# Kernel optimization log

Measured on AMD Instinct MI355X. Metric: run time of the kernel, lower is better.

The kernel has to match this reference:

```python
import jax, jax.numpy as jnp
import numpy as np

B, S, D = 2, 2048, 1024
H = 16
DH = D // H  # 64


def setup_inputs() -> dict:
    key = jax.random.key(0)
    ks = jax.random.split(key, 5)
    scale = 0.02
    x = jax.random.normal(ks[0], (B, S, D), dtype=jnp.float32)
    W_qkv = jax.random.normal(ks[1], (D, 3 * D), dtype=jnp.float32) * scale
    b_qkv = jnp.zeros((3 * D,), dtype=jnp.float32)
    W_out = jax.random.normal(ks[2], (D, D), dtype=jnp.float32) * scale
    b_out = jnp.zeros((D,), dtype=jnp.float32)
    return {"x": x, "W_qkv": W_qkv, "b_qkv": b_qkv, "W_out": W_out, "b_out": b_out}


def reference(x, W_qkv, b_qkv, W_out, b_out):
    # Fused QKV projection: [B,S,D] @ [D,3D] -> [B,S,3D]
    qkv = jnp.einsum('bsd,df->bsf', x, W_qkv) + b_qkv
    q, k, v = qkv[:, :, :D], qkv[:, :, D:2 * D], qkv[:, :, 2 * D:]
    # Split heads: [B,S,D] -> [B,H,S,DH]
    def split(t):
        return t.reshape(B, S, H, DH).transpose(0, 2, 1, 3)
    q, k, v = split(q), split(k), split(v)
    # Scaled dot-product attention (naive, full score matrix as in source)
    scores = jnp.einsum('bhqd,bhkd->bhqk', q, k) / jnp.sqrt(jnp.float32(DH))
    probs = jax.nn.softmax(scores, axis=-1)  # mask=None, dropout eval-mode identity
    attn = jnp.einsum('bhqk,bhkd->bhqd', probs, v)
    # Merge heads: [B,H,S,DH] -> [B,S,D]
    attn = attn.transpose(0, 2, 1, 3).reshape(B, S, D)
    out = jnp.einsum('bsd,de->bse', attn, W_out) + b_out
    return out
```

## Files before the change

### kernel.cpp

```cpp
#include <hip/hip_runtime.h>

typedef _Float16 half8  __attribute__((ext_vector_type(8)));
typedef _Float16 half4  __attribute__((ext_vector_type(4)));
typedef float    floatx4  __attribute__((ext_vector_type(4)));
typedef float    floatx16 __attribute__((ext_vector_type(16)));
typedef unsigned int uint4v __attribute__((ext_vector_type(4)));

constexpr int B_ = 2, S_ = 2048, D_ = 1024, H_ = 16, M_ = 4096;
constexpr int NR_ = B_ * H_ * S_;
constexpr float QSCALE = 0.18033688011112042f;
constexpr int KVB = 64;
constexpr int HT = 16;

__device__ __forceinline__ void gload16(const void* g, void* l) {
  __builtin_amdgcn_global_load_lds((const __attribute__((address_space(1))) void*)g,
                                   (__attribute__((address_space(3))) void*)l, 16, 0, 0);
}

__global__ __launch_bounds__(256) void cast_f32_f16(const float* __restrict__ in,
                                                    _Float16* __restrict__ out, int n8) {
  int i = blockIdx.x * 256 + threadIdx.x;
  if (i >= n8) return;
  float4 a = reinterpret_cast<const float4*>(in)[2 * i];
  float4 b = reinterpret_cast<const float4*>(in)[2 * i + 1];
  half8 h;
  h[0] = (_Float16)a.x; h[1] = (_Float16)a.y; h[2] = (_Float16)a.z; h[3] = (_Float16)a.w;
  h[4] = (_Float16)b.x; h[5] = (_Float16)b.y; h[6] = (_Float16)b.z; h[7] = (_Float16)b.w;
  reinterpret_cast<half8*>(out)[i] = h;
}

__global__ __launch_bounds__(256) void transpose_cast2(const float* __restrict__ W0,
                                                       _Float16* __restrict__ WT0,
                                                       const float* __restrict__ W1,
                                                       _Float16* __restrict__ WT1) {
  __shared__ float Ws[64][65];
  const int z = blockIdx.z;
  const int NW = z ? D_ : 3 * D_;
  if (blockIdx.x * 64 >= NW) return;
  const float* W = z ? W1 : W0;
  _Float16* WT = z ? WT1 : WT0;
  const int K = D_, N = NW;
  const int n0 = blockIdx.x * 64, k0 = blockIdx.y * 64;
  const int t = threadIdx.x;
#pragma unroll
  for (int i = 0; i < 4; i++) {
    int idx = t + 256 * i;
    int r = idx >> 4, c4 = idx & 15;
    float4 v = *reinterpret_cast<const float4*>(W + (size_t)(k0 + r) * N + n0 + c4 * 4);
    Ws[r][c4 * 4 + 0] = v.x; Ws[r][c4 * 4 + 1] = v.y;
    Ws[r][c4 * 4 + 2] = v.z; Ws[r][c4 * 4 + 3] = v.w;
  }
  __syncthreads();
#pragma unroll
  for (int i = 0; i < 2; i++) {
    int idx = t + 256 * i;
    int r = idx >> 3, ck = idx & 7;
    half8 h;
#pragma unroll
    for (int j = 0; j < 8; j++) h[j] = (_Float16)Ws[ck * 8 + j][r];
    *reinterpret_cast<half8*>(WT + (size_t)(n0 + r) * K + k0 + ck * 8) = h;
  }
}

__global__ __launch_bounds__(512, 2) void gemm256_mfma(
    const _Float16* __restrict__ A, const _Float16* __restrict__ BT,
    const float* __restrict__ bias, _Float16* __restrict__ Cout,
    _Float16* __restrict__ Vt,
    int M, int N, int K, float scale_lo, int ncut) {
  extern __shared__ char smem[];
  const int tid = threadIdx.x, w = tid >> 6, lane = tid & 63;
  const int wm = w >> 1, wn = w & 1;

  const int nwg = gridDim.x, cpx = nwg >> 3;
  const int wg = (blockIdx.x & 7) * cpx + (blockIdx.x >> 3);
  const int nbx = N / 192;
  const int bx = wg % nbx, by = wg / nbx;
  const int m0 = by * 256, n0 = bx * 192;

  const int NT = K >> 6;

  const int rS = tid >> 3, cS = (tid & 7) ^ (rS & 7);
  const char* Apn = (const char*)(A + (size_t)(m0 + rS) * K + cS * 8);
  const char* Bpn = (const char*)(BT + (size_t)(n0 + rS) * K + cS * 8);
  const size_t strideI = (size_t)64 * K * 2;

  auto stageA1 = [&](int buf, int i) {
    gload16(Apn + i * strideI, smem + buf * 32768 + tid * 16 + i * 8192);
  };
  auto stageB1 = [&](int buf, int i) {
    gload16(Bpn + i * strideI, smem + 65536 + buf * 24576 + tid * 16 + i * 8192);
  };

  floatx4 acc[4][6] = {};

#pragma unroll
  for (int i = 0; i < 4; i++) stageA1(0, i);
#pragma unroll
  for (int i = 0; i < 3; i++) stageB1(0, i);
  Apn += 128; Bpn += 128;

  for (int kt = 0; kt < NT; ++kt) {
    const int p = kt & 1;
    asm volatile("s_waitcnt vmcnt(0)" ::: "memory");
    __builtin_amdgcn_s_barrier();
    __builtin_amdgcn_sched_barrier(0);

    const char* Ab = smem + p * 32768;
    const char* Bb = smem + 65536 + p * 24576;
    const bool more = (kt + 1 < NT);

    half8 bf[6][2];
#pragma unroll
    for (int n = 0; n < 6; n++)
#pragma unroll
      for (int ks = 0; ks < 2; ks++) {
        int row = wn * 96 + n * 16 + (lane & 15);
        int ch = (ks * 4 + (lane >> 4)) ^ (row & 7);
        bf[n][ks] = *reinterpret_cast<const half8*>(Bb + row * 128 + ch * 16);
      }

#pragma unroll
    for (int q = 0; q < 4; q++) {
      half8 af[2];
#pragma unroll
      for (int ks = 0; ks < 2; ks++) {
        int row = wm * 64 + q * 16 + (lane & 15);
        int ch = (ks * 4 + (lane >> 4)) ^ (row & 7);
        af[ks] = *reinterpret_cast<const half8*>(Ab + row * 128 + ch * 16);
      }
      if (more) {
        if (q == 0)      { stageA1(p ^ 1, 0); stageA1(p ^ 1, 1); }
        else if (q == 1) { stageA1(p ^ 1, 2); stageA1(p ^ 1, 3); }
        else if (q == 2) { stageB1(p ^ 1, 0); stageB1(p ^ 1, 1); }
        else             { stageB1(p ^ 1, 2); }
      }
      __builtin_amdgcn_s_setprio(1);
#pragma unroll
      for (int ks = 0; ks < 2; ks++)
#pragma unroll
        for (int n = 0; n < 6; n++)
          acc[q][n] = __builtin_amdgcn_mfma_f32_16x16x32_f16(
              af[ks], bf[n][ks], acc[q][n], 0, 0, 0);
      __builtin_amdgcn_s_setprio(0);
    }
    Apn += 128; Bpn += 128;
    __builtin_amdgcn_sched_barrier(0);
    __builtin_amdgcn_s_barrier();
  }

#pragma unroll
  for (int mf = 0; mf < 4; mf++)
#pragma unroll
    for (int n = 0; n < 6; n++) {
      int col = n0 + wn * 96 + n * 16 + (lane & 15);
      float bv = bias[col];
      float sc = (col < ncut) ? scale_lo : 1.0f;
      int row0 = m0 + wm * 64 + mf * 16 + (lane >> 4) * 4;
      half4 hv;
#pragma unroll
      for (int reg = 0; reg < 4; reg++) {
        float v = (acc[mf][n][reg] + bv) * sc;
        _Float16 hvv = (_Float16)v;
        Cout[(size_t)(row0 + reg) * N + col] = hvv;
        hv[reg] = hvv;
      }
      if (col >= 2 * D_) {
        int d = col - 2 * D_;
        int bb = row0 >> 11, s0 = row0 & 2047;
        _Float16* vt = Vt + ((size_t)(bb * H_ + (d >> 6)) * 64 + (d & 63)) * S_ + s0;
        *reinterpret_cast<half4*>(vt) = hv;
      }
    }
}

__global__ __launch_bounds__(256, 2) void gemm128_mfma(
    const _Float16* __restrict__ A, const _Float16* __restrict__ BT,
    const float* __restrict__ bias, float* __restrict__ Cout,
    int M, int N, int K) {
  extern __shared__ char smem[];
  const int tid = threadIdx.x, w = tid >> 6, lane = tid & 63;
  const int wm = w >> 1, wn = w & 1;

  const int nwg = gridDim.x, cpx = nwg >> 3;
  const int wg = (blockIdx.x & 7) * cpx + (blockIdx.x >> 3);
  const int nbx = N >> 7;
  const int bx = wg % nbx, by = wg / nbx;
  const int m0 = by * 128, n0 = bx * 128;

  const int NT = K >> 6;

  const int rS = tid >> 3, cS = (tid & 7) ^ (rS & 7);
  const char* Apn = (const char*)(A + (size_t)(m0 + rS) * K + cS * 8);
  const char* Bpn = (const char*)(BT + (size_t)(n0 + rS) * K + cS * 8);
  const size_t strideI = (size_t)32 * K * 2;

  auto stageA1 = [&](int buf, int i) {
    gload16(Apn + i * strideI, smem + buf * 16384 + tid * 16 + i * 4096);
  };
  auto stageB1 = [&](int buf, int i) {
    gload16(Bpn + i * strideI, smem + 32768 + buf * 16384 + tid * 16 + i * 4096);
  };

  floatx4 acc[4][4] = {};

#pragma unroll
  for (int i = 0; i < 4; i++) stageA1(0, i);
#pragma unroll
  for (int i = 0; i < 4; i++) stageB1(0, i);
  Apn += 128; Bpn += 128;

  for (int kt = 0; kt < NT; ++kt) {
    const int p = kt & 1;
    asm volatile("s_waitcnt vmcnt(0)" ::: "memory");
    __builtin_amdgcn_s_barrier();
    __builtin_amdgcn_sched_barrier(0);

    const char* Ab = smem + p * 16384;
    const char* Bb = smem + 32768 + p * 16384;
    const bool more = (kt + 1 < NT);

    half8 bf[4][2];
#pragma unroll
    for (int n = 0; n < 4; n++)
#pragma unroll
      for (int ks = 0; ks < 2; ks++) {
        int row = wn * 64 + n * 16 + (lane & 15);
        int ch = (ks * 4 + (lane >> 4)) ^ (row & 7);
        bf[n][ks] = *reinterpret_cast<const half8*>(Bb + row * 128 + ch * 16);
      }

#pragma unroll
    for (int q = 0; q < 4; q++) {
      half8 af[2];
#pragma unroll
      for (int ks = 0; ks < 2; ks++) {
        int row = wm * 64 + q * 16 + (lane & 15);
        int ch = (ks * 4 + (lane >> 4)) ^ (row & 7);
        af[ks] = *reinterpret_cast<const half8*>(Ab + row * 128 + ch * 16);
      }
      if (more) {
        if (q == 0)      { stageA1(p ^ 1, 0); stageA1(p ^ 1, 1); }
        else if (q == 1) { stageA1(p ^ 1, 2); stageA1(p ^ 1, 3); }
        else if (q == 2) { stageB1(p ^ 1, 0); stageB1(p ^ 1, 1); }
        else             { stageB1(p ^ 1, 2); stageB1(p ^ 1, 3); }
      }
      __builtin_amdgcn_s_setprio(1);
#pragma unroll
      for (int ks = 0; ks < 2; ks++)
#pragma unroll
        for (int n = 0; n < 4; n++)
          acc[q][n] = __builtin_amdgcn_mfma_f32_16x16x32_f16(
              af[ks], bf[n][ks], acc[q][n], 0, 0, 0);
      __builtin_amdgcn_s_setprio(0);
    }
    Apn += 128; Bpn += 128;
    __builtin_amdgcn_sched_barrier(0);
    __builtin_amdgcn_s_barrier();
  }

#pragma unroll
  for (int q = 0; q < 4; q++)
#pragma unroll
    for (int n = 0; n < 4; n++) {
      int col = n0 + wn * 64 + n * 16 + (lane & 15);
      float bv = bias[col];
#pragma unroll
      for (int reg = 0; reg < 4; reg++) {
        int row = m0 + wm * 64 + q * 16 + (lane >> 4) * 4 + reg;
        Cout[(size_t)row * N + col] = acc[q][n][reg] + bv;
      }
    }
}

__global__ __launch_bounds__(256, 4) void flash_mfma(const _Float16* __restrict__ qkv,
                                                     const _Float16* __restrict__ Vt,
                                                     _Float16* __restrict__ Opart,
                                                     float* __restrict__ keys) {
  const int qt = blockIdx.x, h = blockIdx.y;
  const int b = blockIdx.z >> 1, sp = blockIdx.z & 1;
  const int t = threadIdx.x, w = t >> 6, lane = t & 63;
  const int lo = lane & 31, hi = lane >> 5;

  __shared__ _Float16 Ks[2][KVB * 64];
  __shared__ _Float16 Vts[2][64 * KVB];

  const int qrow = qt * 128 + w * 32 + lo;
  const _Float16* qbase = qkv + (size_t)(b * S_ + qrow) * (3 * D_) + h * 64;
  half8 qf[4];
#pragma unroll
  for (int kd = 0; kd < 4; kd++)
    qf[kd] = *reinterpret_cast<const half8*>(qbase + kd * 16 + hi * 8);
  asm volatile("" : "+v"(qf[0]), "+v"(qf[1]), "+v"(qf[2]), "+v"(qf[3]));

  const size_t kbase = (size_t)(b * S_) * (3 * D_) + D_ + h * 64;
  const size_t vbase = (size_t)(b * H_ + h) * 64 * S_;
  const int kvbase = sp * (S_ / 2);

  const int rs = t >> 3, cs = (t & 7) ^ (rs & 7);
  const char* kp = (const char*)(qkv + kbase + (size_t)(kvbase + rs) * (3 * D_) + cs * 8);
  const char* vp = (const char*)(Vt + vbase + (size_t)rs * S_ + kvbase + cs * 8);
  constexpr size_t K_ROW32 = (size_t)32 * 3 * D_ * 2;
  constexpr size_t V_ROW32 = (size_t)32 * S_ * 2;
  constexpr size_t K_TILE  = (size_t)KVB * 3 * D_ * 2;
  constexpr size_t V_TILE  = (size_t)KVB * 2;

  auto stage = [&](int buf) {
    char* kd_ = (char*)&Ks[buf][0] + t * 16;
    char* vd_ = (char*)&Vts[buf][0] + t * 16;
    gload16(kp, kd_);
    gload16(kp + K_ROW32, kd_ + 4096);
    gload16(vp, vd_);
    gload16(vp + V_ROW32, vd_ + 4096);
  };

  floatx16 o0, o1;
#pragma unroll
  for (int r = 0; r < 16; r++) { o0[r] = 0.f; o1[r] = 0.f; }
  float m = -1e30f, l = 0.f;

  stage(0);
  kp += K_TILE; vp += V_TILE;

#pragma unroll 2
  for (int tt = 0; tt < HT; ++tt) {
    const int cb = tt & 1;
    if (tt + 1 < HT) {
      stage(cb ^ 1);
      kp += K_TILE; vp += V_TILE;
      asm volatile("s_waitcnt vmcnt(4)" ::: "memory");
    } else {
      asm volatile("s_waitcnt vmcnt(0)" ::: "memory");
    }
    __builtin_amdgcn_s_barrier();
    __builtin_amdgcn_sched_barrier(0);

    const char* kb2 = (const char*)&Ks[cb][0];
    floatx16 s0v, s1v;
#pragma unroll
    for (int r = 0; r < 16; r++) { s0v[r] = 0.f; s1v[r] = 0.f; }
    __builtin_amdgcn_s_setprio(1);
#pragma unroll
    for (int kd = 0; kd < 4; kd++) {
      int r0 = lo, r1 = 32 + lo;
      half8 k0f = *reinterpret_cast<const half8*>(
          kb2 + r0 * 128 + (((kd * 2 + hi) ^ (r0 & 7)) * 16));
      half8 k1f = *reinterpret_cast<const half8*>(
          kb2 + r1 * 128 + (((kd * 2 + hi) ^ (r1 & 7)) * 16));
      s0v = __builtin_amdgcn_mfma_f32_32x32x16_f16(k0f, qf[kd], s0v, 0, 0, 0);
      s1v = __builtin_amdgcn_mfma_f32_32x32x16_f16(k1f, qf[kd], s1v, 0, 0, 0);
    }
    __builtin_amdgcn_s_setprio(0);

    float tm[16];
#pragma unroll
    for (int r = 0; r < 16; r++) tm[r] = fmaxf(s0v[r], s1v[r]);
    float u0 = fmaxf(fmaxf(tm[0], tm[1]), tm[2]);
    float u1 = fmaxf(fmaxf(tm[3], tm[4]), tm[5]);
    float u2 = fmaxf(fmaxf(tm[6], tm[7]), tm[8]);
    float u3 = fmaxf(fmaxf(tm[9], tm[10]), tm[11]);
    float u4 = fmaxf(fmaxf(tm[12], tm[13]), tm[14]);
    float pm = fmaxf(fmaxf(u0, u1), u2);
    pm = fmaxf(fmaxf(pm, u3), u4);
    pm = fmaxf(pm, tm[15]);
    pm = fmaxf(pm, __shfl_xor(pm, 32));
    if (!__all(pm <= m + 8.0f)) {
      float mn = fmaxf(m, pm);
      float al = __builtin_amdgcn_exp2f(m - mn);
      m = mn; l *= al;
#pragma unroll
      for (int r = 0; r < 16; r++) { o0[r] *= al; o1[r] *= al; }
    }
    float rr[16];
#pragma unroll
    for (int r = 0; r < 16; r++) {
      s0v[r] = __builtin_amdgcn_exp2f(s0v[r] - m);
      s1v[r] = __builtin_amdgcn_exp2f(s1v[r] - m);
      rr[r] = s0v[r] + s1v[r];
    }
#pragma unroll
    for (int st = 8; st >= 1; st >>= 1)
#pragma unroll
      for (int r = 0; r < st; r++) rr[r] += rr[r + st];
    float rs2 = rr[0];
    rs2 += __shfl_xor(rs2, 32);
    l += rs2;

    half8 pf0a, pf0b, pf1a, pf1b;
    {
      unsigned a0 = __builtin_bit_cast(unsigned, __builtin_amdgcn_cvt_pkrtz(s0v[0], s0v[1]));
      unsigned b0 = __builtin_bit_cast(unsigned, __builtin_amdgcn_cvt_pkrtz(s0v[4], s0v[5]));
      unsigned a1 = __builtin_bit_cast(unsigned, __builtin_amdgcn_cvt_pkrtz(s0v[2], s0v[3]));
      unsigned b1 = __builtin_bit_cast(unsigned, __builtin_amdgcn_cvt_pkrtz(s0v[6], s0v[7]));
      asm("v_permlane32_swap_b32 %0, %1" : "+v"(a0), "+v"(b0));
      asm("v_permlane32_swap_b32 %0, %1" : "+v"(a1), "+v"(b1));
      uint4v u; u[0] = a0; u[1] = a1; u[2] = b0; u[3] = b1;
      pf0a = __builtin_bit_cast(half8, u);
      a0 = __builtin_bit_cast(unsigned, __builtin_amdgcn_cvt_pkrtz(s0v[8], s0v[9]));
      b0 = __builtin_bit_cast(unsigned, __builtin_amdgcn_cvt_pkrtz(s0v[12], s0v[13]));
      a1 = __builtin_bit_cast(unsigned, __builtin_amdgcn_cvt_pkrtz(s0v[10], s0v[11]));
      b1 = __builtin_bit_cast(unsigned, __builtin_amdgcn_cvt_pkrtz(s0v[14], s0v[15]));
      asm("v_permlane32_swap_b32 %0, %1" : "+v"(a0), "+v"(b0));
      asm("v_permlane32_swap_b32 %0, %1" : "+v"(a1), "+v"(b1));
      u[0] = a0; u[1] = a1; u[2] = b0; u[3] = b1;
      pf0b = __builtin_bit_cast(half8, u);
      a0 = __builtin_bit_cast(unsigned, __builtin_amdgcn_cvt_pkrtz(s1v[0], s1v[1]));
      b0 = __builtin_bit_cast(unsigned, __builtin_amdgcn_cvt_pkrtz(s1v[4], s1v[5]));
      a1 = __builtin_bit_cast(unsigned, __builtin_amdgcn_cvt_pkrtz(s1v[2], s1v[3]));
      b1 = __builtin_bit_cast(unsigned, __builtin_amdgcn_cvt_pkrtz(s1v[6], s1v[7]));
      asm("v_permlane32_swap_b32 %0, %1" : "+v"(a0), "+v"(b0));
      asm("v_permlane32_swap_b32 %0, %1" : "+v"(a1), "+v"(b1));
      u[0] = a0; u[1] = a1; u[2] = b0; u[3] = b1;
      pf1a = __builtin_bit_cast(half8, u);
      a0 = __builtin_bit_cast(unsigned, __builtin_amdgcn_cvt_pkrtz(s1v[8], s1v[9]));
      b0 = __builtin_bit_cast(unsigned, __builtin_amdgcn_cvt_pkrtz(s1v[12], s1v[13]));
      a1 = __builtin_bit_cast(unsigned, __builtin_amdgcn_cvt_pkrtz(s1v[10], s1v[11]));
      b1 = __builtin_bit_cast(unsigned, __builtin_amdgcn_cvt_pkrtz(s1v[14], s1v[15]));
      asm("v_permlane32_swap_b32 %0, %1" : "+v"(a0), "+v"(b0));
      asm("v_permlane32_swap_b32 %0, %1" : "+v"(a1), "+v"(b1));
      u[0] = a0; u[1] = a1; u[2] = b0; u[3] = b1;
      pf1b = __builtin_bit_cast(half8, u);
    }

    const char* vb2 = (const char*)&Vts[cb][0];
    __builtin_amdgcn_s_setprio(1);
#pragma unroll
    for (int ks = 0; ks < 4; ks++) {
      half8 pf = (ks == 0) ? pf0a : (ks == 1) ? pf0b : (ks == 2) ? pf1a : pf1b;
      const int ch = ks * 2 + hi;
      half8 vf0 = *reinterpret_cast<const half8*>(vb2 + lo * 128 + ((ch ^ (lo & 7)) * 16));
      half8 vf1 = *reinterpret_cast<const half8*>(vb2 + (lo + 32) * 128 + ((ch ^ (lo & 7)) * 16));
      o0 = __builtin_amdgcn_mfma_f32_32x32x16_f16(vf0, pf, o0, 0, 0, 0);
      o1 = __builtin_amdgcn_mfma_f32_32x32x16_f16(vf1, pf, o1, 0, 0, 0);
    }
    __builtin_amdgcn_s_setprio(0);

    __builtin_amdgcn_sched_barrier(0);
    __builtin_amdgcn_s_barrier();
  }

  float inv = 1.0f / l;
  const int gr = (b * H_ + h) * S_ + qrow;
  _Float16* ob = Opart + ((size_t)sp * NR_ + gr) * 64;
#pragma unroll
  for (int mt = 0; mt < 2; mt++)
#pragma unroll
    for (int rq = 0; rq < 4; rq++) {
      half4 v;
#pragma unroll
      for (int e = 0; e < 4; e++) v[e] = (_Float16)(((mt ? o1 : o0)[4 * rq + e]) * inv);
      *reinterpret_cast<half4*>(ob + 32 * mt + 8 * rq + 4 * hi) = v;
    }
  if (hi == 0) keys[sp * NR_ + gr] = m + __log2f(l);
}

__global__ __launch_bounds__(256) void flash_combine(const _Float16* __restrict__ Opart,
                                                     const float* __restrict__ keys,
                                                     _Float16* __restrict__ attn_out) {
  const int gr = blockIdx.x * 256 + threadIdx.x;
  const float k0 = keys[gr], k1 = keys[NR_ + gr];
  const float mx = fmaxf(k0, k1);
  const float w0 = __builtin_amdgcn_exp2f(k0 - mx);
  const float w1 = __builtin_amdgcn_exp2f(k1 - mx);
  const float inv = 1.0f / (w0 + w1);
  const float a0 = w0 * inv, a1 = w1 * inv;
  const int bh = gr >> 11, qs = gr & 2047, b = bh >> 4, h = bh & 15;
  const half8* p0 = reinterpret_cast<const half8*>(Opart + (size_t)gr * 64);
  const half8* p1 = reinterpret_cast<const half8*>(Opart + ((size_t)NR_ + gr) * 64);
  half8* ob = reinterpret_cast<half8*>(
      attn_out + ((size_t)(b * S_ + qs)) * D_ + h * 64);
#pragma unroll
  for (int j = 0; j < 8; j++) {
    half8 x0 = p0[j], x1 = p1[j];
    half8 o;
#pragma unroll
    for (int e = 0; e < 8; e++)
      o[e] = (_Float16)(a0 * (float)x0[e] + a1 * (float)x1[e]);
    ob[j] = o;
  }
}

extern "C" void kernel_launch(void* const* d_in, const int* in_sizes, int n_in,
                              void* d_out, int out_size, void* d_ws, size_t ws_size,
                              hipStream_t stream) {
  const float* x     = (const float*)d_in[0];
  const float* W_qkv = (const float*)d_in[1];
  const float* b_qkv = (const float*)d_in[2];
  const float* W_out = (const float*)d_in[3];
  const float* b_out = (const float*)d_in[4];
  float* out = (float*)d_out;

  _Float16* xh    = (_Float16*)d_ws;
  _Float16* qkvh  = xh + (size_t)M_ * D_;
  _Float16* Vth   = qkvh + (size_t)M_ * 3 * D_;
  _Float16* WoT   = Vth + (size_t)B_ * H_ * 64 * S_;
  _Float16* WqT   = WoT + (size_t)D_ * D_;
  _Float16* Opart = WqT;
  float*    keys  = (float*)(Opart + (size_t)2 * NR_ * 64);
  _Float16* atth  = xh;

  cast_f32_f16<<<(M_ * D_ / 8 + 255) / 256, 256, 0, stream>>>(x, xh, M_ * D_ / 8);
  transpose_cast2<<<dim3(3 * D_ / 64, D_ / 64, 2), 256, 0, stream>>>(
      W_qkv, WqT, W_out, WoT);

  gemm256_mfma<<<256, 512, 114688, stream>>>(
      xh, WqT, b_qkv, qkvh, Vth, M_, 3 * D_, D_, QSCALE, D_);

  flash_mfma<<<dim3(S_ / 128, H_, B_ * 2), 256, 0, stream>>>(qkvh, Vth, Opart, keys);

  flash_combine<<<NR_ / 256, 256, 0, stream>>>(Opart, keys, atth);

  gemm128_mfma<<<256, 256, 65536, stream>>>(
      atth, WoT, b_out, out, M_, D_, D_);
}
```

Before: 124.9 us.

## Fuse split-KV flash combine into output projection GEMM A-tile loading

```diff
diff --git a/kernel.cpp b/kernel.cpp
--- a/kernel.cpp
+++ b/kernel.cpp
@@ -174,7 +174,8 @@
 }
 
 __global__ __launch_bounds__(256, 2) void gemm128_mfma(
-    const _Float16* __restrict__ A, const _Float16* __restrict__ BT,
+    const _Float16* __restrict__ Opart, const float* __restrict__ keys,
+    const _Float16* __restrict__ BT,
     const float* __restrict__ bias, float* __restrict__ Cout,
     int M, int N, int K) {
   extern __shared__ char smem[];
@@ -190,12 +191,27 @@
   const int NT = K >> 6;
 
   const int rS = tid >> 3, cS = (tid & 7) ^ (rS & 7);
-  const char* Apn = (const char*)(A + (size_t)(m0 + rS) * K + cS * 8);
   const char* Bpn = (const char*)(BT + (size_t)(n0 + rS) * K + cS * 8);
   const size_t strideI = (size_t)32 * K * 2;
 
-  auto stageA1 = [&](int buf, int i) {
-    gload16(Apn + i * strideI, smem + buf * 16384 + tid * 16 + i * 4096);
+  const int rAb = (m0 + rS) >> 11;
+  const int rAs = (m0 + rS) & 2047;
+
+  auto stageA1 = [&](int buf, int kt, int i) {
+    int gr = (rAb * 16 + kt) * 2048 + rAs + 32 * i;
+    float k0 = keys[gr], k1 = keys[NR_ + gr];
+    float mx = fmaxf(k0, k1);
+    float w0 = __builtin_amdgcn_exp2f(k0 - mx);
+    float w1 = __builtin_amdgcn_exp2f(k1 - mx);
+    float inv = 1.0f / (w0 + w1);
+    float a0 = w0 * inv, a1 = w1 * inv;
+    half8 x0 = *reinterpret_cast<const half8*>(Opart + (size_t)gr * 64 + cS * 8);
+    half8 x1 = *reinterpret_cast<const half8*>(Opart + ((size_t)NR_ + gr) * 64 + cS * 8);
+    half8 o;
+#pragma unroll
+    for (int j = 0; j < 8; j++)
+      o[j] = (_Float16)(a0 * (float)x0[j] + a1 * (float)x1[j]);
+    *reinterpret_cast<half8*>(smem + buf * 16384 + tid * 16 + i * 4096) = o;
   };
   auto stageB1 = [&](int buf, int i) {
     gload16(Bpn + i * strideI, smem + 32768 + buf * 16384 + tid * 16 + i * 4096);
@@ -204,10 +220,11 @@
   floatx4 acc[4][4] = {};
 
 #pragma unroll
-  for (int i = 0; i < 4; i++) stageA1(0, i);
+  for (int i = 0; i < 4; i++) stageA1(0, 0, i);
 #pragma unroll
   for (int i = 0; i < 4; i++) stageB1(0, i);
-  Apn += 128; Bpn += 128;
+  Bpn += 128;
+  asm volatile("s_waitcnt lgkmcnt(0)" ::: "memory");
 
   for (int kt = 0; kt < NT; ++kt) {
     const int p = kt & 1;
@@ -239,8 +256,8 @@
         af[ks] = *reinterpret_cast<const half8*>(Ab + row * 128 + ch * 16);
       }
       if (more) {
-        if (q == 0)      { stageA1(p ^ 1, 0); stageA1(p ^ 1, 1); }
-        else if (q == 1) { stageA1(p ^ 1, 2); stageA1(p ^ 1, 3); }
+        if (q == 0)      { stageA1(p ^ 1, kt + 1, 0); stageA1(p ^ 1, kt + 1, 1); }
+        else if (q == 1) { stageA1(p ^ 1, kt + 1, 2); stageA1(p ^ 1, kt + 1, 3); }
         else if (q == 2) { stageB1(p ^ 1, 0); stageB1(p ^ 1, 1); }
         else             { stageB1(p ^ 1, 2); stageB1(p ^ 1, 3); }
       }
@@ -253,7 +270,8 @@
               af[ks], bf[n][ks], acc[q][n], 0, 0, 0);
       __builtin_amdgcn_s_setprio(0);
     }
-    Apn += 128; Bpn += 128;
+    Bpn += 128;
+    asm volatile("s_waitcnt lgkmcnt(0)" ::: "memory");
     __builtin_amdgcn_sched_barrier(0);
     __builtin_amdgcn_s_barrier();
   }
@@ -453,32 +471,6 @@
   if (hi == 0) keys[sp * NR_ + gr] = m + __log2f(l);
 }
 
-__global__ __launch_bounds__(256) void flash_combine(const _Float16* __restrict__ Opart,
-                                                     const float* __restrict__ keys,
-                                                     _Float16* __restrict__ attn_out) {
-  const int gr = blockIdx.x * 256 + threadIdx.x;
-  const float k0 = keys[gr], k1 = keys[NR_ + gr];
-  const float mx = fmaxf(k0, k1);
-  const float w0 = __builtin_amdgcn_exp2f(k0 - mx);
-  const float w1 = __builtin_amdgcn_exp2f(k1 - mx);
-  const float inv = 1.0f / (w0 + w1);
-  const float a0 = w0 * inv, a1 = w1 * inv;
-  const int bh = gr >> 11, qs = gr & 2047, b = bh >> 4, h = bh & 15;
-  const half8* p0 = reinterpret_cast<const half8*>(Opart + (size_t)gr * 64);
-  const half8* p1 = reinterpret_cast<const half8*>(Opart + ((size_t)NR_ + gr) * 64);
-  half8* ob = reinterpret_cast<half8*>(
-      attn_out + ((size_t)(b * S_ + qs)) * D_ + h * 64);
-#pragma unroll
-  for (int j = 0; j < 8; j++) {
-    half8 x0 = p0[j], x1 = p1[j];
-    half8 o;
-#pragma unroll
-    for (int e = 0; e < 8; e++)
-      o[e] = (_Float16)(a0 * (float)x0[e] + a1 * (float)x1[e]);
-    ob[j] = o;
-  }
-}
-
 extern "C" void kernel_launch(void* const* d_in, const int* in_sizes, int n_in,
                               void* d_out, int out_size, void* d_ws, size_t ws_size,
                               hipStream_t stream) {
@@ -496,7 +488,6 @@
   _Float16* WqT   = WoT + (size_t)D_ * D_;
   _Float16* Opart = WqT;
   float*    keys  = (float*)(Opart + (size_t)2 * NR_ * 64);
-  _Float16* atth  = xh;
 
   cast_f32_f16<<<(M_ * D_ / 8 + 255) / 256, 256, 0, stream>>>(x, xh, M_ * D_ / 8);
   transpose_cast2<<<dim3(3 * D_ / 64, D_ / 64, 2), 256, 0, stream>>>(
@@ -507,8 +498,6 @@
 
   flash_mfma<<<dim3(S_ / 128, H_, B_ * 2), 256, 0, stream>>>(qkvh, Vth, Opart, keys);
 
-  flash_combine<<<NR_ / 256, 256, 0, stream>>>(Opart, keys, atth);
-
   gemm128_mfma<<<256, 256, 65536, stream>>>(
-      atth, WoT, b_out, out, M_, D_, D_);
-}
+      Opart, keys, WoT, b_out, out, M_, D_, D_);
+}
```

Measured after the change: 142.3 us. +13.9%, slower.
